# Performance work log

Hardware: AMD Instinct MI355X
Metric: run time of the kernel (lower is better)

Reference implementation:

```python
import jax, jax.numpy as jnp
import numpy as np

NF, VOCAB, E, ST, L, BATCH = 39, 10000, 128, 16, 4, 2048
SEQ = NF + 1  # cls token + fields


def setup_inputs() -> dict:
    key = jax.random.key(0)
    ks = jax.random.split(key, 16)
    se = 1.0 / np.sqrt(E)
    s2e = 1.0 / np.sqrt(2 * E)
    inp = {
        "x": jax.random.randint(ks[0], (BATCH, NF), 0, VOCAB),
        "emb_table": jax.random.normal(ks[1], (NF, VOCAB + 1, E), jnp.float32) * 0.02,
        "cls_token": jax.random.normal(ks[2], (1, 1, E), jnp.float32) * 0.02,
        "ln_g": jnp.ones((L, 2, E), jnp.float32),
        "ln_b": jnp.zeros((L, 2, E), jnp.float32),
        "xproj_w": jax.random.normal(ks[3], (L, 2, E, 2 * E), jnp.float32) * se,
        "xproj_b": jnp.zeros((L, 2, 2 * E), jnp.float32),
        "A": jax.random.uniform(ks[4], (L, 2, E, ST), jnp.float32, -0.01, 0.01),
        "D": jnp.ones((L, 2, E), jnp.float32),
        "outproj_w": jax.random.normal(ks[5], (L, 2, E, E), jnp.float32) * se,
        "outproj_b": jnp.zeros((L, 2, E), jnp.float32),
        "merge_w": jax.random.normal(ks[6], (L, 2 * E, E), jnp.float32) * s2e,
        "merge_b": jnp.zeros((L, E), jnp.float32),
        "w1": jax.random.normal(ks[7], (E, 128), jnp.float32) * se,
        "b1": jnp.zeros((128,), jnp.float32),
        "w2": jax.random.normal(ks[8], (128, 64), jnp.float32) * (1.0 / np.sqrt(128)),
        "b2": jnp.zeros((64,), jnp.float32),
        "w3": jax.random.normal(ks[9], (64, 1), jnp.float32) * 0.125,
        "b3": jnp.zeros((1,), jnp.float32),
    }
    return inp


def _layernorm(x, g, b, eps=1e-5):
    m = x.mean(-1, keepdims=True)
    v = ((x - m) ** 2).mean(-1, keepdims=True)
    return (x - m) * jax.lax.rsqrt(v + eps) * g + b


def _mamba_block(x, g, bb, wx, bx, A, D, wo, bo):
    # x: [b, s, e]
    res = x
    xn = _layernorm(x, g, bb)
    xp = xn @ wx + bx                       # [b, s, 2e]
    delta, Bm = jnp.split(xp, 2, axis=-1)
    delta = jax.nn.softplus(delta)
    # torch: h = cumsum(xn*B)[...,None]; out = (h * exp(delta[...,None]*A)).sum(-1)
    # equivalent: out = cumsum(xn*B) * exp(delta[...,None]*A).sum(-1)
    s = jnp.exp(delta[..., None] * A).sum(-1)   # [b, s, e] (4D intermediate [b,s,e,st])
    h = jnp.cumsum(xn * Bm, axis=1)             # [b, s, e]
    out = h * s + xn * D
    return out @ wo + bo + res


def _forward(x, emb_table, cls_token, ln_g, ln_b, xproj_w, xproj_b, A, D,
             outproj_w, outproj_b, merge_w, merge_b, w1, b1, w2, b2, w3, b3):
    batch = x.shape[0]
    emb = emb_table.at[:, 0, :].set(0.0)        # padding_idx=0 rows zeroed
    seq = emb[jnp.arange(NF)[None, :], x]       # [b, nf, e]
    cls = jnp.broadcast_to(cls_token, (batch, 1, E))
    seq = jnp.concatenate([cls, seq], axis=1)   # [b, nf+1, e]

    def body(carry, p):
        g, bb, wx, bx, Ap, Dp, wo, bo, mw, mb = p
        f = _mamba_block(carry, g[0], bb[0], wx[0], bx[0], Ap[0], Dp[0], wo[0], bo[0])
        bk = _mamba_block(carry[:, ::-1], g[1], bb[1], wx[1], bx[1],
                          Ap[1], Dp[1], wo[1], bo[1])[:, ::-1]
        out = jnp.concatenate([f, bk], axis=-1) @ mw + mb
        return out, None

    seq, _ = jax.lax.scan(body, seq, (ln_g, ln_b, xproj_w, xproj_b, A, D,
                                      outproj_w, outproj_b, merge_w, merge_b))
    h = seq[:, 0, :]
    h = jax.nn.relu(h @ w1 + b1)
    h = jax.nn.relu(h @ w2 + b2)
    return (h @ w3 + b3)[:, 0]                  # [batch] logits


def reference(x, emb_table, cls_token, ln_g, ln_b, xproj_w, xproj_b, A, D,
              outproj_w, outproj_b, merge_w, merge_b, w1, b1, w2, b2, w3, b3):
    return _forward(x, emb_table, cls_token, ln_g, ln_b, xproj_w, xproj_b, A, D,
                    outproj_w, outproj_b, merge_w, merge_b, w1, b1, w2, b2, w3, b3)
```

## Files before the change

kernel.cpp:

```cpp
#include <hip/hip_runtime.h>

#define NFEAT   39
#define SEQL    40
#define EDIM    128
#define NSTATE  16
#define NLAYERS 4
#define VROWS   10001

typedef __attribute__((ext_vector_type(8))) short short8;
typedef __attribute__((ext_vector_type(4))) float f32x4;

__device__ __forceinline__ float b2f(unsigned short u) {
  unsigned v = ((unsigned)u) << 16;
  return __builtin_bit_cast(float, v);
}
__device__ __forceinline__ unsigned short f2b(float f) {
  unsigned u = __builtin_bit_cast(unsigned, f);
  u += 0x7FFFu + ((u >> 16) & 1u);
  return (unsigned short)(u >> 16);
}
__device__ __forceinline__ float ldin(const void* p, long i, int bf) {
  if (bf) return b2f(((const unsigned short*)p)[i]);
  return ((const float*)p)[i];
}

#define OFF_CLS 0
#define OFF_LNG 128
#define OFF_LNB 1152
#define OFF_XB  2176
#define OFF_AC  4224
#define OFF_D   8320
#define OFF_OB  9344
#define OFF_MB  10368
#define OFF_W1  10880
#define OFF_B1  27264
#define OFF_W2  27392
#define OFF_B2  35584
#define OFF_W3  35648
#define OFF_B3  35712
#define NF32    35713

#define NPK_XW  262144
#define NPK_V   65536

struct SrcPtrs { const void* p[19]; };

__global__ void convert_kernel(SrcPtrs sp, float* W, unsigned short* pkxw,
                               unsigned short* pkv0, unsigned short* pkv1,
                               unsigned short* pkmr, int* flag) {
  unsigned w0 = *(const unsigned*)sp.p[3];
  int bf = (w0 != 0x3F800000u) ? 1 : 0;
  if (blockIdx.x == 0 && threadIdx.x == 0) *flag = bf;
  const int T0 = NF32;
  const int T1 = T0 + NPK_XW;
  const int T2 = T1 + NPK_V;
  const int T3 = T2 + NPK_V;
  const int T4 = T3 + NPK_V;
  for (int i = blockIdx.x * blockDim.x + threadIdx.x; i < T4;
       i += gridDim.x * blockDim.x) {
    if (i < T0) {
      if (i >= OFF_AC && i < OFF_D) {
        int o  = i - OFF_AC;
        int c  = o & 3;
        int e  = (o >> 2) & 127;
        int pd = o >> 9;
        float acc = 0.f;
        for (int k = 0; k < 16; ++k) {
          float a = ldin(sp.p[7], (pd * 128 + e) * 16 + k, bf);
          float p = a;
          if (c >= 1) p *= a;
          if (c >= 2) p *= a;
          if (c >= 3) p *= a;
          acc += p;
        }
        const float inv = (c == 0) ? 1.f : (c == 1) ? 0.5f
                        : (c == 2) ? (1.f / 6.f) : (1.f / 24.f);
        W[i] = acc * inv;
      } else if (i >= OFF_XB && i < OFF_AC) {
        int o = i - OFF_XB;
        int pd = o >> 8, n = o & 255;
        float acc = ldin(sp.p[6], o, bf);
        for (int k = 0; k < 128; ++k) {
          float bbk = ldin(sp.p[4], pd * 128 + k, bf);
          float wxk = ldin(sp.p[5], ((long)(pd * 128 + k)) * 256 + n, bf);
          acc = fmaf(bbk, wxk, acc);
        }
        W[i] = acc;
      } else if (i >= OFF_MB && i < OFF_W1) {
        int o = i - OFF_MB;
        int l = o >> 7, n = o & 127;
        float acc = ldin(sp.p[12], o, bf);
        for (int k = 0; k < 128; ++k) {
          float bo0 = ldin(sp.p[10], (l * 2) * 128 + k, bf);
          float bo1 = ldin(sp.p[10], (l * 2 + 1) * 128 + k, bf);
          float mwt = ldin(sp.p[11], ((long)(l * 256 + k)) * 128 + n, bf);
          float mwb = ldin(sp.p[11], ((long)(l * 256 + 128 + k)) * 128 + n, bf);
          acc = fmaf(bo0, mwt, fmaf(bo1, mwb, acc));
        }
        W[i] = acc;
      } else {
        const void* s; int li;
        if      (i < OFF_LNG) { s = sp.p[2];  li = i - OFF_CLS; }
        else if (i < OFF_LNB) { s = sp.p[3];  li = i - OFF_LNG; }
        else if (i < OFF_XB)  { s = sp.p[4];  li = i - OFF_LNB; }
        else if (i < OFF_OB)  { s = sp.p[8];  li = i - OFF_D; }
        else if (i < OFF_MB)  { s = sp.p[10]; li = i - OFF_OB; }
        else if (i < OFF_B1)  { s = sp.p[13]; li = i - OFF_W1; }
        else if (i < OFF_W2)  { s = sp.p[14]; li = i - OFF_B1; }
        else if (i < OFF_B2)  { s = sp.p[15]; li = i - OFF_W2; }
        else if (i < OFF_W3)  { s = sp.p[16]; li = i - OFF_B2; }
        else if (i < OFF_B3)  { s = sp.p[17]; li = i - OFF_W3; }
        else                  { s = sp.p[18]; li = i - OFF_B3; }
        W[i] = ldin(s, li, bf);
      }
    } else if (i < T1) {
      int o = i - T0;
      int j = o & 7, lane = (o >> 3) & 63, kb = (o >> 9) & 3;
      int nt = (o >> 11) & 15, pd = o >> 15;
      int k = kb * 32 + (lane >> 4) * 8 + j;
      int n = nt * 16 + (lane & 15);
      float g = ldin(sp.p[3], pd * 128 + k, bf);
      float v = ldin(sp.p[5], ((long)(pd * 128 + k)) * 256 + n, bf) * g;
      pkxw[o] = f2b(v);
    } else {
      int which = (i < T2) ? 0 : (i < T3) ? 1 : 2;
      int o = i - (which == 0 ? T1 : which == 1 ? T2 : T3);
      int j = o & 7, lane = (o >> 3) & 63, kb = (o >> 9) & 3;
      int nt = (o >> 11) & 7, l = o >> 14;
      int k = kb * 32 + (lane >> 4) * 8 + j;
      int n = nt * 16 + (lane & 15);
      float acc = 0.f;
      if (which == 2) {
        acc = ldin(sp.p[11], ((long)(l * 256 + k)) * 128 + n, bf)
            + ldin(sp.p[11], ((long)(l * 256 + 128 + k)) * 128 + n, bf);
        pkmr[o] = f2b(acc);
      } else {
        int pd = l * 2 + which;
        int mrow0 = l * 256 + which * 128;
        for (int m = 0; m < 128; ++m) {
          float wo = ldin(sp.p[9], ((long)(pd * 128 + k)) * 128 + m, bf);
          float mw = ldin(sp.p[11], ((long)(mrow0 + m)) * 128 + n, bf);
          acc = fmaf(wo, mw, acc);
        }
        if (which == 0) pkv0[o] = f2b(acc); else pkv1[o] = f2b(acc);
      }
    }
  }
}

#define SXB_OFF  0
#define SHO_OFF  10880
#define SF_OFF   21760
#define SCAR_OFF 32640
#define LDS_TOT  53760

__global__ __launch_bounds__(256, 3)
void mamba_kernel(const int* __restrict__ x, const void* __restrict__ emb,
                  const float* __restrict__ W,
                  const unsigned short* __restrict__ pkxw,
                  const unsigned short* __restrict__ pkv0,
                  const unsigned short* __restrict__ pkv1,
                  const unsigned short* __restrict__ pkmr,
                  const int* __restrict__ flagp, void* __restrict__ outp) {
  __shared__ __align__(16) unsigned char sMem[LDS_TOT];
  unsigned short* sXB  = (unsigned short*)(sMem + SXB_OFF);
  unsigned short* sHO  = (unsigned short*)(sMem + SHO_OFF);
  unsigned short* sF   = (unsigned short*)(sMem + SF_OFF);
  float*          sCar = (float*)        (sMem + SCAR_OFF);

  const int b    = blockIdx.x;
  const int tid  = threadIdx.x;
  const int w    = tid >> 6;
  const int lane = tid & 63;
  const int q    = lane >> 4;
  const int li   = lane & 15;
  const int bf   = *flagp;

  for (int i = tid; i < SEQL * EDIM; i += 256) {
    int t = i >> 7, e = i & 127;
    float v;
    if (t == 0) v = W[OFF_CLS + e];
    else {
      int f = t - 1;
      int idx = x[b * NFEAT + f];
      v = (idx == 0) ? 0.f : ldin(emb, ((long)f * VROWS + idx) * EDIM + e, bf);
    }
    sCar[t * 132 + e] = v;
  }
  __syncthreads();

  for (int l = 0; l < NLAYERS; ++l) {
    for (int t = w; t < SEQL; t += 4) {
      float v0 = sCar[t * 132 + lane], v1 = sCar[t * 132 + lane + 64];
      float sum = v0 + v1;
      for (int m = 32; m; m >>= 1) sum += __shfl_xor(sum, m, 64);
      float mean = sum * (1.f / 128.f);
      float d0 = v0 - mean, d1 = v1 - mean;
      float vs = d0 * d0 + d1 * d1;
      for (int m = 32; m; m >>= 1) vs += __shfl_xor(vs, m, 64);
      float inv = rsqrtf(vs * (1.f / 128.f) + 1e-5f);
      sXB[t * 136 + lane]      = f2b(d0 * inv);
      sXB[t * 136 + lane + 64] = f2b(d1 * inv);
    }
    __syncthreads();

    for (int dir = 0; dir < 2; ++dir) {
      const int pd = l * 2 + dir;
      const float* bx = W + OFF_XB + pd * 256;
      const float* AC = W + OFF_AC + pd * 512;
      const float* gP = W + OFF_LNG + pd * EDIM;
      const float* bP = W + OFF_LNB + pd * EDIM;
      const float* Dp = W + OFF_D  + pd * EDIM;
      unsigned short* dst = dir ? sF : sHO;

      for (int cti = 0; cti < 2; ++cti) {
        const int ct = w + cti * 4;
        const int e  = ct * 16 + li;
        short8 Bd[4], Bb4[4];
#pragma unroll
        for (int kb = 0; kb < 4; ++kb) {
          Bd[kb]  = *(const short8*)(pkxw + (((pd * 16 + ct)     * 4 + kb) * 64 + lane) * 8);
          Bb4[kb] = *(const short8*)(pkxw + (((pd * 16 + ct + 8) * 4 + kb) * 64 + lane) * 8);
        }
        const float4 cv = *(const float4*)(AC + e * 4);
        float bxd = bx[e], bxb = bx[128 + e];
        float gv = gP[e], bbv = bP[e], Dv = Dp[e];
        float sv[3][4], xnv[3][4], pv[3][4];
#pragma unroll
        for (int m = 0; m < 3; ++m) {
          f32x4 aD = {0.f, 0.f, 0.f, 0.f}, aB = {0.f, 0.f, 0.f, 0.f};
#pragma unroll
          for (int kb = 0; kb < 4; ++kb) {
            const short8 afr = *(const short8*)(sXB + (m * 16 + li) * 136 + kb * 32 + q * 8);
            aD = __builtin_amdgcn_mfma_f32_16x16x32_bf16(afr, Bd[kb],  aD, 0, 0, 0);
            aB = __builtin_amdgcn_mfma_f32_16x16x32_bf16(afr, Bb4[kb], aB, 0, 0, 0);
          }
#pragma unroll
          for (int r = 0; r < 4; ++r) {
            int t = m * 16 + q * 4 + r;
            float xd  = aD[r] + bxd;
            float spv = fmaxf(xd, 0.f) + __logf(1.f + __expf(-fabsf(xd)));
            float s = 16.f + spv * (cv.x + spv * (cv.y + spv * (cv.z + spv * cv.w)));
            sv[m][r] = s;
            float xn = fmaf(b2f(sXB[t * 136 + e]), gv, bbv);
            xnv[m][r] = xn;
            float p = xn * (aB[r] + bxb);
            pv[m][r] = (t < SEQL) ? p : 0.f;
          }
        }
        if (dir == 0) {
          float base = 0.f;
#pragma unroll
          for (int m = 0; m < 3; ++m) {
            float p0 = pv[m][0], p1 = p0 + pv[m][1];
            float p2 = p1 + pv[m][2], p3 = p2 + pv[m][3];
            float c  = p3;
            float e1 = __shfl_up(c, 16, 64);
            float e2 = __shfl_up(c, 32, 64);
            float e3 = __shfl_up(c, 48, 64);
            float ex = (q >= 1 ? e1 : 0.f) + (q >= 2 ? e2 : 0.f) + (q >= 3 ? e3 : 0.f);
            float tot = __shfl(ex + c, 48 + li, 64);
            pv[m][0] = base + ex + p0; pv[m][1] = base + ex + p1;
            pv[m][2] = base + ex + p2; pv[m][3] = base + ex + p3;
            base += tot;
          }
        } else {
          float base = 0.f;
#pragma unroll
          for (int m = 2; m >= 0; --m) {
            float p3 = pv[m][3], p2 = p3 + pv[m][2];
            float p1 = p2 + pv[m][1], p0 = p1 + pv[m][0];
            float c  = p0;
            float e1 = __shfl_down(c, 16, 64);
            float e2 = __shfl_down(c, 32, 64);
            float e3 = __shfl_down(c, 48, 64);
            float ex = (q <= 2 ? e1 : 0.f) + (q <= 1 ? e2 : 0.f) + (q <= 0 ? e3 : 0.f);
            float tot = __shfl(ex + c, li, 64);
            pv[m][0] = base + ex + p0; pv[m][1] = base + ex + p1;
            pv[m][2] = base + ex + p2; pv[m][3] = base + ex + p3;
            base += tot;
          }
        }
#pragma unroll
        for (int m = 0; m < 3; ++m)
#pragma unroll
          for (int r = 0; r < 4; ++r) {
            int t = m * 16 + q * 4 + r;
            if (t < SEQL)
              dst[t * 136 + e] = f2b(pv[m][r] * sv[m][r] + xnv[m][r] * Dv);
          }
      }
      __syncthreads();
    }

    for (int i = tid; i < SEQL * EDIM; i += 256) {
      int t = i >> 7, e = i & 127;
      sXB[t * 136 + e] = f2b(sCar[t * 132 + e]);
    }
    __syncthreads();

    {
      const float* mb = W + OFF_MB + l * EDIM;
      for (int nti = 0; nti < 2; ++nti) {
        const int nt = w + nti * 4;
        const int n  = nt * 16 + li;
        short8 B0[4], B1[4], B2[4];
#pragma unroll
        for (int kb = 0; kb < 4; ++kb) {
          B0[kb] = *(const short8*)(pkv0 + (((l * 8 + nt) * 4 + kb) * 64 + lane) * 8);
          B1[kb] = *(const short8*)(pkv1 + (((l * 8 + nt) * 4 + kb) * 64 + lane) * 8);
          B2[kb] = *(const short8*)(pkmr + (((l * 8 + nt) * 4 + kb) * 64 + lane) * 8);
        }
        float mbv = mb[n];
#pragma unroll
        for (int m = 0; m < 3; ++m) {
          f32x4 ac = {0.f, 0.f, 0.f, 0.f};
#pragma unroll
          for (int kb = 0; kb < 4; ++kb) {
            const short8 a0 = *(const short8*)(sHO + (m * 16 + li) * 136 + kb * 32 + q * 8);
            ac = __builtin_amdgcn_mfma_f32_16x16x32_bf16(a0, B0[kb], ac, 0, 0, 0);
          }
#pragma unroll
          for (int kb = 0; kb < 4; ++kb) {
            const short8 a1 = *(const short8*)(sF + (m * 16 + li) * 136 + kb * 32 + q * 8);
            ac = __builtin_amdgcn_mfma_f32_16x16x32_bf16(a1, B1[kb], ac, 0, 0, 0);
          }
#pragma unroll
          for (int kb = 0; kb < 4; ++kb) {
            const short8 a2 = *(const short8*)(sXB + (m * 16 + li) * 136 + kb * 32 + q * 8);
            ac = __builtin_amdgcn_mfma_f32_16x16x32_bf16(a2, B2[kb], ac, 0, 0, 0);
          }
#pragma unroll
          for (int r = 0; r < 4; ++r) {
            int t = m * 16 + q * 4 + r;
            if (t < SEQL) sCar[t * 132 + n] = ac[r] + mbv;
          }
        }
      }
    }
    __syncthreads();
  }

  if (tid < 128) {
    float a = W[OFF_B1 + tid];
    const float* w1p = W + OFF_W1;
    for (int e = 0; e < EDIM; e += 4) {
      float4 hv = *(const float4*)&sCar[e];
      a = fmaf(hv.x, w1p[(e + 0) * 128 + tid],
          fmaf(hv.y, w1p[(e + 1) * 128 + tid],
          fmaf(hv.z, w1p[(e + 2) * 128 + tid],
          fmaf(hv.w, w1p[(e + 3) * 128 + tid], a))));
    }
    sCar[132 + tid] = fmaxf(a, 0.f);
  }
  __syncthreads();
  if (tid < 64) {
    float a = W[OFF_B2 + tid];
    const float* w2p = W + OFF_W2;
    for (int i = 0; i < 128; ++i) a = fmaf(sCar[132 + i], w2p[i * 64 + tid], a);
    a = fmaxf(a, 0.f);
    float v = a * W[OFF_W3 + tid];
    for (int m = 32; m; m >>= 1) v += __shfl_xor(v, m, 64);
    if (tid == 0) {
      float res = v + W[OFF_B3];
      if (bf) ((unsigned short*)outp)[b] = f2b(res);
      else    ((float*)outp)[b] = res;
    }
  }
}

extern "C" void kernel_launch(void* const* d_in, const int* in_sizes, int n_in,
                              void* d_out, int out_size, void* d_ws, size_t ws_size,
                              hipStream_t stream) {
  (void)in_sizes; (void)n_in; (void)out_size; (void)ws_size;

  SrcPtrs sp;
  for (int k = 0; k < 19; ++k) sp.p[k] = d_in[k];

  int*            flag = (int*)d_ws;
  float*          Wf   = (float*)((char*)d_ws + 256);
  unsigned short* pkxw = (unsigned short*)((char*)d_ws + 256 + 200704);
  unsigned short* pkv0 = pkxw + NPK_XW;
  unsigned short* pkv1 = pkv0 + NPK_V;
  unsigned short* pkmr = pkv1 + NPK_V;

  convert_kernel<<<dim3(512), dim3(256), 0, stream>>>(sp, Wf, pkxw, pkv0, pkv1, pkmr, flag);
  mamba_kernel<<<dim3(2048), dim3(256), 0, stream>>>(
      (const int*)d_in[0], d_in[1], Wf, pkxw, pkv0, pkv1, pkmr, flag, d_out);
}
```

Measured before the change: 566.1 us.

## Fold D-skip term into merge GEMM and store carry in bf16 to shrink LDS

The xn*D skip term is folded algebraically into a new precomputed packed weight (g*D applied through the out-projection and merge), and the constant ln_b*D becomes a bias. The merge GEMM is split per direction and accumulated in registers, so the second per-direction output buffer is no longer needed. The fp32 residual carry is replaced by a bf16 buffer. Together these cut LDS from about 53.7KB to about 34.8KB and raise launch bounds to 4 blocks per CU. The cost is extra precision loss from keeping the residual stream in bf16, plus an additional packed-weight precompute in the convert kernel.

```diff
diff --git a/kernel.cpp b/kernel.cpp
--- a/kernel.cpp
+++ b/kernel.cpp
@@ -47,7 +47,8 @@
 
 __global__ void convert_kernel(SrcPtrs sp, float* W, unsigned short* pkxw,
                                unsigned short* pkv0, unsigned short* pkv1,
-                               unsigned short* pkmr, int* flag) {
+                               unsigned short* pkmr, unsigned short* pkmx,
+                               int* flag) {
   unsigned w0 = *(const unsigned*)sp.p[3];
   int bf = (w0 != 0x3F800000u) ? 1 : 0;
   if (blockIdx.x == 0 && threadIdx.x == 0) *flag = bf;
@@ -56,7 +57,8 @@
   const int T2 = T1 + NPK_V;
   const int T3 = T2 + NPK_V;
   const int T4 = T3 + NPK_V;
-  for (int i = blockIdx.x * blockDim.x + threadIdx.x; i < T4;
+  const int T5 = T4 + NPK_V;
+  for (int i = blockIdx.x * blockDim.x + threadIdx.x; i < T5;
        i += gridDim.x * blockDim.x) {
     if (i < T0) {
       if (i >= OFF_AC && i < OFF_D) {
@@ -86,6 +88,9 @@
           acc = fmaf(bbk, wxk, acc);
         }
         W[i] = acc;
+      } else if (i >= OFF_D && i < OFF_OB) {
+        int o = i - OFF_D;
+        W[i] = ldin(sp.p[4], o, bf) * ldin(sp.p[8], o, bf);
       } else if (i >= OFF_MB && i < OFF_W1) {
         int o = i - OFF_MB;
         int l = o >> 7, n = o & 127;
@@ -103,7 +108,6 @@
         if      (i < OFF_LNG) { s = sp.p[2];  li = i - OFF_CLS; }
         else if (i < OFF_LNB) { s = sp.p[3];  li = i - OFF_LNG; }
         else if (i < OFF_XB)  { s = sp.p[4];  li = i - OFF_LNB; }
-        else if (i < OFF_OB)  { s = sp.p[8];  li = i - OFF_D; }
         else if (i < OFF_MB)  { s = sp.p[10]; li = i - OFF_OB; }
         else if (i < OFF_B1)  { s = sp.p[13]; li = i - OFF_W1; }
         else if (i < OFF_W2)  { s = sp.p[14]; li = i - OFF_B1; }
@@ -123,20 +127,33 @@
       float v = ldin(sp.p[5], ((long)(pd * 128 + k)) * 256 + n, bf) * g;
       pkxw[o] = f2b(v);
     } else {
-      int which = (i < T2) ? 0 : (i < T3) ? 1 : 2;
-      int o = i - (which == 0 ? T1 : which == 1 ? T2 : T3);
+      int which = (i < T2) ? 0 : (i < T3) ? 1 : (i < T4) ? 2 : 3;
+      int o = i - (which == 0 ? T1 : which == 1 ? T2 : which == 2 ? T3 : T4);
       int j = o & 7, lane = (o >> 3) & 63, kb = (o >> 9) & 3;
       int nt = (o >> 11) & 7, l = o >> 14;
       int k = kb * 32 + (lane >> 4) * 8 + j;
       int n = nt * 16 + (lane & 15);
-      float acc = 0.f;
       if (which == 2) {
-        acc = ldin(sp.p[11], ((long)(l * 256 + k)) * 128 + n, bf)
-            + ldin(sp.p[11], ((long)(l * 256 + 128 + k)) * 128 + n, bf);
+        float acc = ldin(sp.p[11], ((long)(l * 256 + k)) * 128 + n, bf)
+                  + ldin(sp.p[11], ((long)(l * 256 + 128 + k)) * 128 + n, bf);
         pkmr[o] = f2b(acc);
+      } else if (which == 3) {
+        float gd0 = ldin(sp.p[3], (l * 2) * 128 + k, bf)
+                  * ldin(sp.p[8], (l * 2) * 128 + k, bf);
+        float gd1 = ldin(sp.p[3], (l * 2 + 1) * 128 + k, bf)
+                  * ldin(sp.p[8], (l * 2 + 1) * 128 + k, bf);
+        float a0 = 0.f, a1 = 0.f;
+        for (int m = 0; m < 128; ++m) {
+          float wo0 = ldin(sp.p[9], ((long)((l * 2) * 128 + k)) * 128 + m, bf);
+          float wo1 = ldin(sp.p[9], ((long)((l * 2 + 1) * 128 + k)) * 128 + m, bf);
+          a0 = fmaf(wo0, ldin(sp.p[11], ((long)(l * 256 + m)) * 128 + n, bf), a0);
+          a1 = fmaf(wo1, ldin(sp.p[11], ((long)(l * 256 + 128 + m)) * 128 + n, bf), a1);
+        }
+        pkmx[o] = f2b(gd0 * a0 + gd1 * a1);
       } else {
         int pd = l * 2 + which;
         int mrow0 = l * 256 + which * 128;
+        float acc = 0.f;
         for (int m = 0; m < 128; ++m) {
           float wo = ldin(sp.p[9], ((long)(pd * 128 + k)) * 128 + m, bf);
           float mw = ldin(sp.p[11], ((long)(mrow0 + m)) * 128 + n, bf);
@@ -148,25 +165,27 @@
   }
 }
 
-#define SXB_OFF  0
-#define SHO_OFF  10880
-#define SF_OFF   21760
-#define SCAR_OFF 32640
-#define LDS_TOT  53760
-
-__global__ __launch_bounds__(256, 3)
+#define SC_OFF  0
+#define SX_OFF  10880
+#define SO_OFF  21760
+#define LDS_TOT 34816
+
+#define AFRAG(base, m, kb) \
+  (*(const short8*)((base) + ((m) * 16 + li) * 136 + (kb) * 32 + q * 8))
+
+__global__ __launch_bounds__(256, 4)
 void mamba_kernel(const int* __restrict__ x, const void* __restrict__ emb,
                   const float* __restrict__ W,
                   const unsigned short* __restrict__ pkxw,
                   const unsigned short* __restrict__ pkv0,
                   const unsigned short* __restrict__ pkv1,
                   const unsigned short* __restrict__ pkmr,
+                  const unsigned short* __restrict__ pkmx,
                   const int* __restrict__ flagp, void* __restrict__ outp) {
   __shared__ __align__(16) unsigned char sMem[LDS_TOT];
-  unsigned short* sXB  = (unsigned short*)(sMem + SXB_OFF);
-  unsigned short* sHO  = (unsigned short*)(sMem + SHO_OFF);
-  unsigned short* sF   = (unsigned short*)(sMem + SF_OFF);
-  float*          sCar = (float*)        (sMem + SCAR_OFF);
+  unsigned short* sC = (unsigned short*)(sMem + SC_OFF);
+  unsigned short* sX = (unsigned short*)(sMem + SX_OFF);
+  unsigned short* sO = (unsigned short*)(sMem + SO_OFF);
 
   const int b    = blockIdx.x;
   const int tid  = threadIdx.x;
@@ -185,13 +204,14 @@
       int idx = x[b * NFEAT + f];
       v = (idx == 0) ? 0.f : ldin(emb, ((long)f * VROWS + idx) * EDIM + e, bf);
     }
-    sCar[t * 132 + e] = v;
+    sC[t * 136 + e] = f2b(v);
   }
   __syncthreads();
 
   for (int l = 0; l < NLAYERS; ++l) {
     for (int t = w; t < SEQL; t += 4) {
-      float v0 = sCar[t * 132 + lane], v1 = sCar[t * 132 + lane + 64];
+      unsigned pr = *(const unsigned*)(sC + t * 136 + 2 * lane);
+      float v0 = b2f((unsigned short)pr), v1 = b2f((unsigned short)(pr >> 16));
       float sum = v0 + v1;
       for (int m = 32; m; m >>= 1) sum += __shfl_xor(sum, m, 64);
       float mean = sum * (1.f / 128.f);
@@ -199,10 +219,18 @@
       float vs = d0 * d0 + d1 * d1;
       for (int m = 32; m; m >>= 1) vs += __shfl_xor(vs, m, 64);
       float inv = rsqrtf(vs * (1.f / 128.f) + 1e-5f);
-      sXB[t * 136 + lane]      = f2b(d0 * inv);
-      sXB[t * 136 + lane + 64] = f2b(d1 * inv);
+      float x0 = d0 * inv, x1 = d1 * inv;
+      unsigned r;
+      asm("v_cvt_pk_bf16_f32 %0, %1, %2" : "=v"(r) : "v"(x0), "v"(x1));
+      *(unsigned*)(sX + t * 136 + 2 * lane) = r;
     }
     __syncthreads();
+
+    f32x4 acc[2][3];
+#pragma unroll
+    for (int a = 0; a < 2; ++a)
+#pragma unroll
+      for (int m = 0; m < 3; ++m) acc[a][m] = (f32x4){0.f, 0.f, 0.f, 0.f};
 
     for (int dir = 0; dir < 2; ++dir) {
       const int pd = l * 2 + dir;
@@ -210,8 +238,7 @@
       const float* AC = W + OFF_AC + pd * 512;
       const float* gP = W + OFF_LNG + pd * EDIM;
       const float* bP = W + OFF_LNB + pd * EDIM;
-      const float* Dp = W + OFF_D  + pd * EDIM;
-      unsigned short* dst = dir ? sF : sHO;
+      const float* bD = W + OFF_D  + pd * EDIM;
 
       for (int cti = 0; cti < 2; ++cti) {
         const int ct = w + cti * 4;
@@ -224,14 +251,14 @@
         }
         const float4 cv = *(const float4*)(AC + e * 4);
         float bxd = bx[e], bxb = bx[128 + e];
-        float gv = gP[e], bbv = bP[e], Dv = Dp[e];
-        float sv[3][4], xnv[3][4], pv[3][4];
+        float gv = gP[e], bbv = bP[e], bdv = bD[e];
+        float sv[3][4], pv[3][4];
 #pragma unroll
         for (int m = 0; m < 3; ++m) {
           f32x4 aD = {0.f, 0.f, 0.f, 0.f}, aB = {0.f, 0.f, 0.f, 0.f};
 #pragma unroll
           for (int kb = 0; kb < 4; ++kb) {
-            const short8 afr = *(const short8*)(sXB + (m * 16 + li) * 136 + kb * 32 + q * 8);
+            const short8 afr = AFRAG(sX, m, kb);
             aD = __builtin_amdgcn_mfma_f32_16x16x32_bf16(afr, Bd[kb],  aD, 0, 0, 0);
             aB = __builtin_amdgcn_mfma_f32_16x16x32_bf16(afr, Bb4[kb], aB, 0, 0, 0);
           }
@@ -242,8 +269,7 @@
             float spv = fmaxf(xd, 0.f) + __logf(1.f + __expf(-fabsf(xd)));
             float s = 16.f + spv * (cv.x + spv * (cv.y + spv * (cv.z + spv * cv.w)));
             sv[m][r] = s;
-            float xn = fmaf(b2f(sXB[t * 136 + e]), gv, bbv);
-            xnv[m][r] = xn;
+            float xn = fmaf(b2f(sX[t * 136 + e]), gv, bbv);
             float p = xn * (aB[r] + bxb);
             pv[m][r] = (t < SEQL) ? p : 0.f;
           }
@@ -287,77 +313,78 @@
           for (int r = 0; r < 4; ++r) {
             int t = m * 16 + q * 4 + r;
             if (t < SEQL)
-              dst[t * 136 + e] = f2b(pv[m][r] * sv[m][r] + xnv[m][r] * Dv);
+              sO[t * 136 + e] = f2b(fmaf(pv[m][r], sv[m][r], bdv));
           }
       }
       __syncthreads();
-    }
-
-    for (int i = tid; i < SEQL * EDIM; i += 256) {
-      int t = i >> 7, e = i & 127;
-      sXB[t * 136 + e] = f2b(sCar[t * 132 + e]);
-    }
-    __syncthreads();
-
-    {
-      const float* mb = W + OFF_MB + l * EDIM;
-      for (int nti = 0; nti < 2; ++nti) {
-        const int nt = w + nti * 4;
-        const int n  = nt * 16 + li;
-        short8 B0[4], B1[4], B2[4];
-#pragma unroll
-        for (int kb = 0; kb < 4; ++kb) {
-          B0[kb] = *(const short8*)(pkv0 + (((l * 8 + nt) * 4 + kb) * 64 + lane) * 8);
-          B1[kb] = *(const short8*)(pkv1 + (((l * 8 + nt) * 4 + kb) * 64 + lane) * 8);
-          B2[kb] = *(const short8*)(pkmr + (((l * 8 + nt) * 4 + kb) * 64 + lane) * 8);
-        }
-        float mbv = mb[n];
-#pragma unroll
-        for (int m = 0; m < 3; ++m) {
-          f32x4 ac = {0.f, 0.f, 0.f, 0.f};
+
+      if (dir == 0) {
+        for (int nti = 0; nti < 2; ++nti) {
+          const int nt = w + nti * 4;
+          short8 B0[4], Bx[4], Br[4];
 #pragma unroll
           for (int kb = 0; kb < 4; ++kb) {
-            const short8 a0 = *(const short8*)(sHO + (m * 16 + li) * 136 + kb * 32 + q * 8);
-            ac = __builtin_amdgcn_mfma_f32_16x16x32_bf16(a0, B0[kb], ac, 0, 0, 0);
-          }
-#pragma unroll
-          for (int kb = 0; kb < 4; ++kb) {
-            const short8 a1 = *(const short8*)(sF + (m * 16 + li) * 136 + kb * 32 + q * 8);
-            ac = __builtin_amdgcn_mfma_f32_16x16x32_bf16(a1, B1[kb], ac, 0, 0, 0);
-          }
-#pragma unroll
-          for (int kb = 0; kb < 4; ++kb) {
-            const short8 a2 = *(const short8*)(sXB + (m * 16 + li) * 136 + kb * 32 + q * 8);
-            ac = __builtin_amdgcn_mfma_f32_16x16x32_bf16(a2, B2[kb], ac, 0, 0, 0);
-          }
-#pragma unroll
-          for (int r = 0; r < 4; ++r) {
-            int t = m * 16 + q * 4 + r;
-            if (t < SEQL) sCar[t * 132 + n] = ac[r] + mbv;
-          }
-        }
+            B0[kb] = *(const short8*)(pkv0 + (((l * 8 + nt) * 4 + kb) * 64 + lane) * 8);
+            Bx[kb] = *(const short8*)(pkmx + (((l * 8 + nt) * 4 + kb) * 64 + lane) * 8);
+            Br[kb] = *(const short8*)(pkmr + (((l * 8 + nt) * 4 + kb) * 64 + lane) * 8);
+          }
+#pragma unroll
+          for (int m = 0; m < 3; ++m) {
+            f32x4 ac = acc[nti][m];
+#pragma unroll
+            for (int kb = 0; kb < 4; ++kb)
+              ac = __builtin_amdgcn_mfma_f32_16x16x32_bf16(AFRAG(sO, m, kb), B0[kb], ac, 0, 0, 0);
+#pragma unroll
+            for (int kb = 0; kb < 4; ++kb)
+              ac = __builtin_amdgcn_mfma_f32_16x16x32_bf16(AFRAG(sX, m, kb), Bx[kb], ac, 0, 0, 0);
+#pragma unroll
+            for (int kb = 0; kb < 4; ++kb)
+              ac = __builtin_amdgcn_mfma_f32_16x16x32_bf16(AFRAG(sC, m, kb), Br[kb], ac, 0, 0, 0);
+            acc[nti][m] = ac;
+          }
+        }
+        __syncthreads();
+      } else {
+        const float* mb = W + OFF_MB + l * EDIM;
+        for (int nti = 0; nti < 2; ++nti) {
+          const int nt = w + nti * 4;
+          const int n  = nt * 16 + li;
+          short8 B1[4];
+#pragma unroll
+          for (int kb = 0; kb < 4; ++kb)
+            B1[kb] = *(const short8*)(pkv1 + (((l * 8 + nt) * 4 + kb) * 64 + lane) * 8);
+          float mbv = mb[n];
+#pragma unroll
+          for (int m = 0; m < 3; ++m) {
+            f32x4 ac = acc[nti][m];
+#pragma unroll
+            for (int kb = 0; kb < 4; ++kb)
+              ac = __builtin_amdgcn_mfma_f32_16x16x32_bf16(AFRAG(sO, m, kb), B1[kb], ac, 0, 0, 0);
+#pragma unroll
+            for (int r = 0; r < 4; ++r) {
+              int t = m * 16 + q * 4 + r;
+              if (t < SEQL) sC[t * 136 + n] = f2b(ac[r] + mbv);
+            }
+          }
+        }
+        __syncthreads();
       }
     }
-    __syncthreads();
   }
 
+  float* sH = (float*)sX;
   if (tid < 128) {
     float a = W[OFF_B1 + tid];
     const float* w1p = W + OFF_W1;
-    for (int e = 0; e < EDIM; e += 4) {
-      float4 hv = *(const float4*)&sCar[e];
-      a = fmaf(hv.x, w1p[(e + 0) * 128 + tid],
-          fmaf(hv.y, w1p[(e + 1) * 128 + tid],
-          fmaf(hv.z, w1p[(e + 2) * 128 + tid],
-          fmaf(hv.w, w1p[(e + 3) * 128 + tid], a))));
-    }
-    sCar[132 + tid] = fmaxf(a, 0.f);
+    for (int e = 0; e < EDIM; ++e)
+      a = fmaf(b2f(sC[e]), w1p[e * 128 + tid], a);
+    sH[tid] = fmaxf(a, 0.f);
   }
   __syncthreads();
   if (tid < 64) {
     float a = W[OFF_B2 + tid];
     const float* w2p = W + OFF_W2;
-    for (int i = 0; i < 128; ++i) a = fmaf(sCar[132 + i], w2p[i * 64 + tid], a);
+    for (int i = 0; i < 128; ++i) a = fmaf(sH[i], w2p[i * 64 + tid], a);
     a = fmaxf(a, 0.f);
     float v = a * W[OFF_W3 + tid];
     for (int m = 32; m; m >>= 1) v += __shfl_xor(v, m, 64);
@@ -383,8 +410,10 @@
   unsigned short* pkv0 = pkxw + NPK_XW;
   unsigned short* pkv1 = pkv0 + NPK_V;
   unsigned short* pkmr = pkv1 + NPK_V;
-
-  convert_kernel<<<dim3(512), dim3(256), 0, stream>>>(sp, Wf, pkxw, pkv0, pkv1, pkmr, flag);
+  unsigned short* pkmx = pkmr + NPK_V;
+
+  convert_kernel<<<dim3(512), dim3(256), 0, stream>>>(sp, Wf, pkxw, pkv0, pkv1,
+                                                      pkmr, pkmx, flag);
   mamba_kernel<<<dim3(2048), dim3(256), 0, stream>>>(
-      (const int*)d_in[0], d_in[1], Wf, pkxw, pkv0, pkv1, pkmr, flag, d_out);
-}
+      (const int*)d_in[0], d_in[1], Wf, pkxw, pkv0, pkv1, pkmr, pkmx, flag, d_out);
+}
```

New measurement: 677.2 us. 1.2x slower.
